# Kernel optimization log

Measured on AMD Instinct MI355X. Metric: run time of the kernel, lower is better.

The kernel has to match this reference:

```python
import jax, jax.numpy as jnp
import numpy as np

DXV, DRUGV = 10000, 3000
DXANC, DRUGANC = 2000, 600
A = 8            # max ancestors per leaf
ONTOD = 128; EHRD = 128; ATTND = 128; PTATTND = 128; DPL = 500
B, T, DXN, DRUGN = 64, 20, 30, 30


def _l2norm(x):
    n = jnp.sqrt(jnp.sum(x * x, axis=-1, keepdims=True))
    return x / jnp.maximum(n, 1e-12)


def _onto_emb(emb, leaves, ancestors, aW, ab, cW, cb):
    # GRAM-style ontology attention: per leaf, attend over its ancestor set.
    le = emb[leaves]          # (V, A, ONTOD)
    ae = emb[ancestors]       # (V, A, ONTOD)
    s = jnp.tanh(jnp.concatenate([le, ae], -1) @ aW + ab) @ cW + cb  # (V, A, 1)
    attn = jax.nn.softmax(s, axis=1)
    out = jnp.sum(attn * ae, axis=1)                                 # (V, ONTOD)
    pad = jnp.zeros((1, out.shape[1]), out.dtype)                    # padding row at idx V
    return jnp.concatenate([out, pad], axis=0)


def setup_inputs() -> dict:
    key = jax.random.key(0)
    ks = jax.random.split(key, 24)
    s = 0.02
    dxseqs = jax.random.randint(ks[0], (B, T, DXN), 0, DXV + 1)
    drugseqs = jax.random.randint(ks[1], (B, T, DRUGN), 0, DRUGV + 1)
    dx_onehot = jax.random.uniform(ks[2], (T, B, DXV), dtype=jnp.float32)
    drug_onehot = jax.random.uniform(ks[3], (T, B, DRUGV), dtype=jnp.float32)
    dx_leaves = jnp.broadcast_to(jnp.arange(DXV)[:, None], (DXV, A))
    dx_ancestors = jax.random.randint(ks[4], (DXV, A), 0, DXV + DXANC).at[:, 0].set(jnp.arange(DXV))
    drug_leaves = jnp.broadcast_to(jnp.arange(DRUGV)[:, None], (DRUGV, A))
    drug_ancestors = jax.random.randint(ks[5], (DRUGV, A), 0, DRUGV + DRUGANC).at[:, 0].set(jnp.arange(DRUGV))
    ehr_dx_emb = (jax.random.normal(ks[6], (DXV + 1, EHRD)) * s).at[DXV].set(0.0)
    ehr_drug_emb = (jax.random.normal(ks[7], (DRUGV + 1, EHRD)) * s).at[DRUGV].set(0.0)
    return {
        "dxseqs": dxseqs, "drugseqs": drugseqs,
        "dx_onehot": dx_onehot, "drug_onehot": drug_onehot,
        "dx_leaves": dx_leaves, "dx_ancestors": dx_ancestors,
        "drug_leaves": drug_leaves, "drug_ancestors": drug_ancestors,
        "dx_onto_emb": jax.random.normal(ks[8], (DXV + DXANC, ONTOD)) * s,
        "dx_onto_aW": jax.random.normal(ks[9], (2 * ONTOD, ATTND)) * s,
        "dx_onto_ab": jnp.zeros((ATTND,)),
        "dx_onto_cW": jax.random.normal(ks[10], (ATTND, 1)) * s,
        "dx_onto_cb": jnp.zeros((1,)),
        "drug_onto_emb": jax.random.normal(ks[11], (DRUGV + DRUGANC, ONTOD)) * s,
        "drug_onto_aW": jax.random.normal(ks[12], (2 * ONTOD, ATTND)) * s,
        "drug_onto_ab": jnp.zeros((ATTND,)),
        "drug_onto_cW": jax.random.normal(ks[13], (ATTND, 1)) * s,
        "drug_onto_cb": jnp.zeros((1,)),
        "ehr_dx_emb": ehr_dx_emb, "ehr_drug_emb": ehr_drug_emb,
        "co_W": jax.random.normal(ks[14], (EHRD, DXV + DRUGV)) * s,
        "co_b": jnp.zeros((DXV + DRUGV,)),
        "attn_W": jax.random.normal(ks[15], (2 * ONTOD + 2 * EHRD, PTATTND)) * s,
        "attn_b": jnp.zeros((PTATTND,)),
        "comb_W": jax.random.normal(ks[16], (PTATTND, 1)) * s,
        "comb_b": jnp.zeros((1,)),
        "dp_W": jax.random.normal(ks[17], (ONTOD + EHRD, DPL)) * s,
        "dp_b": jnp.zeros((DPL,)),
        "read_W": jax.random.normal(ks[18], (ONTOD + EHRD, 1)) * s,
        "read_b": jnp.zeros((1,)),
    }


def reference(dxseqs, drugseqs, dx_onehot, drug_onehot,
              dx_leaves, dx_ancestors, drug_leaves, drug_ancestors,
              dx_onto_emb, dx_onto_aW, dx_onto_ab, dx_onto_cW, dx_onto_cb,
              drug_onto_emb, drug_onto_aW, drug_onto_ab, drug_onto_cW, drug_onto_cb,
              ehr_dx_emb, ehr_drug_emb, co_W, co_b,
              attn_W, attn_b, comb_W, comb_b, dp_W, dp_b, read_W, read_b):
    dxALL = _onto_emb(dx_onto_emb, dx_leaves, dx_ancestors, dx_onto_aW, dx_onto_ab, dx_onto_cW, dx_onto_cb)      # (DXV+1, ONTOD)
    drugALL = _onto_emb(drug_onto_emb, drug_leaves, drug_ancestors, drug_onto_aW, drug_onto_ab, drug_onto_cW, drug_onto_cb)
    dxE = ehr_dx_emb[dxseqs]                                # (B,T,DXN,EHRD)
    drugE = ehr_drug_emb[drugseqs]                          # (B,T,DRUGN,EHRD)
    EHREmb = jnp.concatenate([dxE, drugE], axis=2)          # (B,T,N,EHRD)
    ontoEmb = jnp.concatenate([dxALL[dxseqs], drugALL[drugseqs]], axis=2)  # (B,T,N,ONTOD)
    EHRVEmb = _l2norm(jnp.sum(dxE, axis=2)) + _l2norm(jnp.sum(drugE, axis=2))  # (B,T,EHRD)
    dxontoV = jnp.einsum('tbv,vd->btd', dx_onehot, dxALL[:-1])
    drugontoV = jnp.einsum('tbv,vd->btd', drug_onehot, drugALL[:-1])
    cooccurU = jax.nn.softmax(EHRVEmb @ co_W + co_b, axis=2)               # (B,T,DXV+DRUGV)
    vonehot = jnp.concatenate([jnp.transpose(dx_onehot, (1, 0, 2)),
                               jnp.transpose(drug_onehot, (1, 0, 2))], axis=2)
    cooccur_loss = -jnp.mean(jnp.sum(vonehot * jnp.log(cooccurU), axis=(1, 2)))
    ontoV = _l2norm(dxontoV) + _l2norm(drugontoV)
    vs = jnp.concatenate([ontoV, EHRVEmb], axis=2)          # (B,T,ONTOD+EHRD)
    dxdrug = jnp.concatenate([EHREmb, ontoEmb], axis=3)     # (B,T,N,EHRD+ONTOD)
    N = dxdrug.shape[2]
    vs_rep = jnp.broadcast_to(vs[:, :, None, :], (vs.shape[0], vs.shape[1], N, vs.shape[2]))
    attnInput = jnp.concatenate([vs_rep, dxdrug], axis=3)   # (B,T,N,2*ONTOD+2*EHRD)
    pre = jnp.tanh(attnInput @ attn_W + attn_b) @ comb_W + comb_b          # (B,T,N,1)
    attn = jax.nn.softmax(pre, axis=2)
    vs2 = jnp.sum(attn * dxdrug, axis=2)                    # (B,T,EHRD+ONTOD)
    vs_dp = _l2norm(vs2)
    DP_result = jax.nn.softmax(jnp.tanh(vs_dp) @ dp_W + dp_b, axis=2)
    read_result = jax.nn.sigmoid(vs_dp @ read_W + read_b)
    return (read_result, DP_result, cooccur_loss * 10.0)
```

## Files before the change

kernel.cpp:

```cpp
#include <hip/hip_runtime.h>
#include <hip/hip_bf16.h>
#include <math.h>

#define BB 64
#define TT 20
#define BT 1280
#define DXV 10000
#define DRUGV 3000
#define COV 13000
#define DPL 500
#define KC 40

typedef __attribute__((ext_vector_type(8))) short short8v;
typedef __attribute__((ext_vector_type(4))) float f32x4;

__device__ __forceinline__ unsigned short f2bf(float f) {
  __hip_bfloat16 h = __float2bfloat16(f);
  return *reinterpret_cast<unsigned short*>(&h);
}

__global__ __launch_bounds__(256, 4) void k_onto(
    const float* __restrict__ emb, const int* __restrict__ leaves, const int* __restrict__ anc,
    const float* __restrict__ aW, const float* __restrict__ ab, const float* __restrict__ cW,
    float* __restrict__ out)
{
  __shared__ __align__(16) float xe[4][128];
  __shared__ __align__(16) float xa[4][8][128];
  __shared__ float part[4][8][2];
  __shared__ float sv[32];
  const int tid = threadIdx.x;
  const int v0 = blockIdx.x * 4;

  for (int i = tid; i < 4*128; i += 256) {
    const int lv = i >> 7, d = i & 127;
    xe[lv][d] = emb[leaves[(v0 + lv)*8] * 128 + d];
  }
  for (int i = tid; i < 32*128; i += 256) {
    const int row = i >> 7, d = i & 127;
    xa[row >> 3][row & 7][d] = emb[anc[(v0 + (row >> 3))*8 + (row & 7)] * 128 + d];
  }
  __syncthreads();

  const int j = tid & 127, half = tid >> 7;

  float ld[4];
  { const float abj = ab[j]; ld[0] = ld[1] = ld[2] = ld[3] = abj; }
  for (int k0 = 0; k0 < 128; k0 += 4) {
    const float w0 = aW[(k0+0)*128 + j];
    const float w1 = aW[(k0+1)*128 + j];
    const float w2 = aW[(k0+2)*128 + j];
    const float w3 = aW[(k0+3)*128 + j];
    #pragma unroll
    for (int lv = 0; lv < 4; ++lv) {
      const float4 x4 = *reinterpret_cast<const float4*>(&xe[lv][k0]);
      ld[lv] = fmaf(x4.x, w0, fmaf(x4.y, w1, fmaf(x4.z, w2, fmaf(x4.w, w3, ld[lv]))));
    }
  }

  float acc[4][4];
  #pragma unroll
  for (int lv = 0; lv < 4; ++lv)
    #pragma unroll
    for (int ai = 0; ai < 4; ++ai) acc[lv][ai] = ld[lv];
  for (int k0 = 0; k0 < 128; k0 += 4) {
    const float w0 = aW[(128+k0+0)*128 + j];
    const float w1 = aW[(128+k0+1)*128 + j];
    const float w2 = aW[(128+k0+2)*128 + j];
    const float w3 = aW[(128+k0+3)*128 + j];
    float4 es[16];
    #pragma unroll
    for (int lv = 0; lv < 4; ++lv)
      #pragma unroll
      for (int ai = 0; ai < 4; ++ai)
        es[lv*4 + ai] = *reinterpret_cast<const float4*>(&xa[lv][half + 2*ai][k0]);
    #pragma unroll
    for (int lv = 0; lv < 4; ++lv)
      #pragma unroll
      for (int ai = 0; ai < 4; ++ai) {
        const float4 e4 = es[lv*4 + ai];
        acc[lv][ai] = fmaf(e4.x, w0, fmaf(e4.y, w1, fmaf(e4.z, w2, fmaf(e4.w, w3, acc[lv][ai]))));
      }
  }

  {
    const float cwj = cW[j];
    #pragma unroll
    for (int lv = 0; lv < 4; ++lv)
      #pragma unroll
      for (int ai = 0; ai < 4; ++ai) {
        float p = tanhf(acc[lv][ai]) * cwj;
        for (int off = 32; off; off >>= 1) p += __shfl_down(p, off);
        if ((tid & 63) == 0) part[lv][half + 2*ai][(tid >> 6) & 1] = p;
      }
  }
  __syncthreads();
  if (tid < 32) sv[tid] = part[tid >> 3][tid & 7][0] + part[tid >> 3][tid & 7][1];
  __syncthreads();
  if (tid < 4) {
    float m = -1e30f;
    #pragma unroll
    for (int a = 0; a < 8; ++a) m = fmaxf(m, sv[tid*8 + a]);
    float e[8], ssum = 0.f;
    #pragma unroll
    for (int a = 0; a < 8; ++a) { e[a] = __expf(sv[tid*8 + a] - m); ssum += e[a]; }
    const float inv = 1.f / ssum;
    #pragma unroll
    for (int a = 0; a < 8; ++a) sv[tid*8 + a] = e[a] * inv;
  }
  __syncthreads();
  #pragma unroll
  for (int it = 0; it < 2; ++it) {
    const int i = it*256 + tid;
    const int lv = i >> 7, d = i & 127;
    float o = 0.f;
    #pragma unroll
    for (int a = 0; a < 8; ++a) o += sv[lv*8 + a] * xa[lv][a][d];
    out[(v0 + lv)*128 + d] = o;
  }
}

__global__ __launch_bounds__(128) void k_ehr(
    const int* __restrict__ dxs, const int* __restrict__ drs,
    const float* __restrict__ edx, const float* __restrict__ edr,
    float* __restrict__ vs)
{
  const int bt = blockIdx.x, d = threadIdx.x;
  float sdx = 0.f, sdr = 0.f;
  for (int n = 0; n < 30; ++n) sdx += edx[dxs[bt*30 + n]*128 + d];
  for (int n = 0; n < 30; ++n) sdr += edr[drs[bt*30 + n]*128 + d];
  __shared__ float red[2][2];
  float p1 = sdx*sdx, p2 = sdr*sdr;
  for (int off = 32; off; off >>= 1) { p1 += __shfl_down(p1, off); p2 += __shfl_down(p2, off); }
  if ((d & 63) == 0) { red[0][d>>6] = p1; red[1][d>>6] = p2; }
  __syncthreads();
  const float n1 = sqrtf(red[0][0] + red[0][1]);
  const float n2 = sqrtf(red[1][0] + red[1][1]);
  vs[bt*256 + 128 + d] = sdx / fmaxf(n1, 1e-12f) + sdr / fmaxf(n2, 1e-12f);
}

__global__ __launch_bounds__(256, 4) void k_einsum(
    const float* __restrict__ oneh, const float* __restrict__ tabl,
    float* __restrict__ outp, int V, int vcount)
{
  __shared__ __align__(16) float As[32][KC];
  __shared__ __align__(16) float Bs[KC][128];
  const int tid = threadIdx.x;
  const int rbase = blockIdx.x * 32;
  const int vbase = blockIdx.y * vcount;
  const int cg = tid & 31, rg = tid >> 5;
  const int d0 = cg * 4, r0 = rg * 4;
  float acc[4][4];
  #pragma unroll
  for (int r = 0; r < 4; ++r)
    #pragma unroll
    for (int q = 0; q < 4; ++q) acc[r][q] = 0.f;

  for (int c0 = 0; c0 < vcount; c0 += KC) {
    __syncthreads();
    for (int i = tid; i < 320; i += 256) {
      const int r = i / 10, q = i % 10;
      const int row = rbase + r;
      const int b = row / TT, t = row % TT;
      *reinterpret_cast<float4*>(&As[r][q*4]) =
          *reinterpret_cast<const float4*>(&oneh[(t*BB + b)*V + vbase + c0 + q*4]);
    }
    for (int i = tid; i < 1280; i += 256) {
      const int rr = i >> 5, q = i & 31;
      *reinterpret_cast<float4*>(&Bs[rr][q*4]) =
          *reinterpret_cast<const float4*>(&tabl[(vbase + c0 + rr)*128 + q*4]);
    }
    __syncthreads();
    #pragma unroll
    for (int kk = 0; kk < KC; kk += 4) {
      const float4 b0 = *reinterpret_cast<const float4*>(&Bs[kk+0][d0]);
      const float4 b1 = *reinterpret_cast<const float4*>(&Bs[kk+1][d0]);
      const float4 b2 = *reinterpret_cast<const float4*>(&Bs[kk+2][d0]);
      const float4 b3 = *reinterpret_cast<const float4*>(&Bs[kk+3][d0]);
      float4 a4[4];
      #pragma unroll
      for (int r = 0; r < 4; ++r) a4[r] = *reinterpret_cast<const float4*>(&As[r0 + r][kk]);
      #pragma unroll
      for (int r = 0; r < 4; ++r) {
        acc[r][0] = fmaf(a4[r].x, b0.x, fmaf(a4[r].y, b1.x, fmaf(a4[r].z, b2.x, fmaf(a4[r].w, b3.x, acc[r][0]))));
        acc[r][1] = fmaf(a4[r].x, b0.y, fmaf(a4[r].y, b1.y, fmaf(a4[r].z, b2.y, fmaf(a4[r].w, b3.y, acc[r][1]))));
        acc[r][2] = fmaf(a4[r].x, b0.z, fmaf(a4[r].y, b1.z, fmaf(a4[r].z, b2.z, fmaf(a4[r].w, b3.z, acc[r][2]))));
        acc[r][3] = fmaf(a4[r].x, b0.w, fmaf(a4[r].y, b1.w, fmaf(a4[r].z, b2.w, fmaf(a4[r].w, b3.w, acc[r][3]))));
      }
    }
  }
  #pragma unroll
  for (int r = 0; r < 4; ++r) {
    const int row = rbase + r0 + r;
    #pragma unroll
    for (int q = 0; q < 4; ++q)
      atomicAdd(&outp[row*128 + d0 + q], acc[r][q]);
  }
}

__global__ __launch_bounds__(128) void k_vs(
    const float* __restrict__ dxo, const float* __restrict__ dro, float* __restrict__ vs)
{
  const int bt = blockIdx.x, d = threadIdx.x;
  const float a = dxo[bt*128 + d], b = dro[bt*128 + d];
  __shared__ float red[2][2];
  float p1 = a*a, p2 = b*b;
  for (int off = 32; off; off >>= 1) { p1 += __shfl_down(p1, off); p2 += __shfl_down(p2, off); }
  if ((d & 63) == 0) { red[0][d>>6] = p1; red[1][d>>6] = p2; }
  __syncthreads();
  const float n1 = sqrtf(red[0][0] + red[0][1]);
  const float n2 = sqrtf(red[1][0] + red[1][1]);
  vs[bt*256 + d] = a / fmaxf(n1, 1e-12f) + b / fmaxf(n2, 1e-12f);
}

__global__ __launch_bounds__(256) void k_cvtco(
    const float* __restrict__ coW, unsigned short* __restrict__ coWbT)
{
  __shared__ float t[32][129];
  const int v0 = blockIdx.x * 32;
  const int tid = threadIdx.x;
  for (int i = tid; i < 128*32; i += 256) {
    const int k = i >> 5, v = i & 31;
    if (v0 + v < COV) t[v][k] = coW[k*COV + v0 + v];
  }
  __syncthreads();
  for (int i = tid; i < 32*128; i += 256) {
    const int v = i >> 7, k = i & 127;
    if (v0 + v < COV) coWbT[(v0 + v)*128 + k] = f2bf(t[v][k]);
  }
}

__global__ __launch_bounds__(256, 4) void k_cooc(
    const float* __restrict__ vs, const unsigned short* __restrict__ coWbT,
    const float* __restrict__ cob,
    const float* __restrict__ dxoh, const float* __restrict__ droh,
    float* __restrict__ es_g, float* __restrict__ od_g, float* __restrict__ os_g)
{
  __shared__ __align__(16) unsigned short Xa[32*128];
  __shared__ float l_es[32], l_od[32], l_os[32];
  const int tid = threadIdx.x;
  const int rbase = blockIdx.x * 32;
  const int nbase = blockIdx.y * 512;
  char* xb = reinterpret_cast<char*>(Xa);

  if (tid < 32) { l_es[tid] = 0.f; l_od[tid] = 0.f; l_os[tid] = 0.f; }
  for (int i = tid; i < 32*32; i += 256) {
    const int r = i >> 5, q = i & 31;
    const float4 v = *reinterpret_cast<const float4*>(&vs[(rbase + r)*256 + 128 + q*4]);
    ushort4 h;
    h.x = f2bf(v.x); h.y = f2bf(v.y); h.z = f2bf(v.z); h.w = f2bf(v.w);
    const int byte = (r*256 + q*8) ^ ((r & 7) << 4);
    *reinterpret_cast<ushort4*>(xb + byte) = h;
  }
  __syncthreads();

  const int lane = tid & 63, w = tid >> 6;
  const int l15 = lane & 15, kg = lane >> 4;
  const int nw = nbase + w*128;
  f32x4 acc[2][8];
  #pragma unroll
  for (int mt = 0; mt < 2; ++mt)
    #pragma unroll
    for (int nt = 0; nt < 8; ++nt) acc[mt][nt] = f32x4{0.f, 0.f, 0.f, 0.f};

  #pragma unroll
  for (int kt = 0; kt < 4; ++kt) {
    short8v a[2];
    #pragma unroll
    for (int mt = 0; mt < 2; ++mt) {
      const int row = mt*16 + l15;
      a[mt] = *reinterpret_cast<const short8v*>(xb + ((row*256 + kt*64 + kg*16) ^ ((row & 7) << 4)));
    }
    #pragma unroll
    for (int nt = 0; nt < 8; ++nt) {
      int ncol = nw + nt*16 + l15;
      if (ncol > COV - 1) ncol = COV - 1;
      const short8v b = *reinterpret_cast<const short8v*>(
          reinterpret_cast<const char*>(coWbT) + ncol*256 + kt*64 + kg*16);
      acc[0][nt] = __builtin_amdgcn_mfma_f32_16x16x32_bf16(a[0], b, acc[0][nt], 0, 0, 0);
      acc[1][nt] = __builtin_amdgcn_mfma_f32_16x16x32_bf16(a[1], b, acc[1][nt], 0, 0, 0);
    }
  }

  #pragma unroll
  for (int mt = 0; mt < 2; ++mt) {
    #pragma unroll
    for (int r = 0; r < 4; ++r) {
      const int lrow = mt*16 + kg*4 + r;
      const int grow = rbase + lrow;
      const int b_ = grow / TT, t_ = grow % TT;
      float es_a = 0.f, od_a = 0.f, os_a = 0.f;
      #pragma unroll
      for (int nt = 0; nt < 8; ++nt) {
        const int v = nw + nt*16 + l15;
        if (v < COV) {
          const float lgv = acc[mt][nt][r] + cob[v];
          const float oh = (v < DXV) ? dxoh[(t_*BB + b_)*DXV + v]
                                     : droh[(t_*BB + b_)*DRUGV + (v - DXV)];
          es_a += __expf(lgv);
          od_a = fmaf(oh, lgv, od_a);
          os_a += oh;
        }
      }
      #pragma unroll
      for (int off = 1; off < 16; off <<= 1) {
        es_a += __shfl_xor(es_a, off);
        od_a += __shfl_xor(od_a, off);
        os_a += __shfl_xor(os_a, off);
      }
      if (l15 == 0) {
        atomicAdd(&l_es[lrow], es_a);
        atomicAdd(&l_od[lrow], od_a);
        atomicAdd(&l_os[lrow], os_a);
      }
    }
  }
  __syncthreads();
  if (tid < 32) {
    atomicAdd(&es_g[rbase + tid], l_es[tid]);
    atomicAdd(&od_g[rbase + tid], l_od[tid]);
    atomicAdd(&os_g[rbase + tid], l_os[tid]);
  }
}

__global__ __launch_bounds__(256) void k_loss(
    const float* __restrict__ es_g, const float* __restrict__ od_g, const float* __restrict__ os_g,
    float* __restrict__ out)
{
  const int tid = threadIdx.x;
  float a = 0.f;
  for (int r = tid; r < BT; r += 256)
    a += logf(es_g[r]) * os_g[r] - od_g[r];
  __shared__ float red[4];
  for (int off = 32; off; off >>= 1) a += __shfl_down(a, off);
  if ((tid & 63) == 0) red[tid >> 6] = a;
  __syncthreads();
  if (tid == 0) out[0] = (red[0] + red[1] + red[2] + red[3]) * (10.f / (float)BB);
}

__global__ __launch_bounds__(128) void k_cvtw(
    const float* __restrict__ aW, unsigned short* __restrict__ aWbT)
{
  const int k = blockIdx.x, n = threadIdx.x;
  aWbT[n*256 + k] = f2bf(aW[(256 + k)*128 + n]);
}

__global__ __launch_bounds__(256, 4) void k_attn(
    const int* __restrict__ dxs, const int* __restrict__ drs,
    const float* __restrict__ edx, const float* __restrict__ edr,
    const float* __restrict__ dxALL, const float* __restrict__ drugALL,
    const float* __restrict__ vs, const float* __restrict__ aW,
    const float* __restrict__ ab, const float* __restrict__ cWc,
    const unsigned short* __restrict__ aWbT,
    float* __restrict__ vsdp)
{
  __shared__ __align__(16) unsigned short X2[64*256];
  __shared__ __align__(16) float vrow[256];
  __shared__ float bp[2][128];
  __shared__ float base[128];
  __shared__ float sattn[64];
  __shared__ int codes[60];
  __shared__ float red[4];
  const int tid = threadIdx.x;
  const int bt = blockIdx.x;
  char* x2b = reinterpret_cast<char*>(X2);

  if (tid < 64) sattn[tid] = 0.f;
  if (tid < 60) codes[tid] = (tid < 30) ? dxs[bt*30 + tid] : drs[bt*30 + tid - 30];
  vrow[tid] = vs[bt*256 + tid];
  __syncthreads();

  for (int idx = tid; idx < 60*64; idx += 256) {
    const int n = idx >> 6, q = idx & 63;
    const float* src = (q < 32) ? ((n < 30) ? edx : edr)
                                : ((n < 30) ? dxALL : drugALL);
    const float4 v = *reinterpret_cast<const float4*>(&src[codes[n]*128 + (q & 31)*4]);
    ushort4 h;
    h.x = f2bf(v.x); h.y = f2bf(v.y); h.z = f2bf(v.z); h.w = f2bf(v.w);
    const int byte = (n*512 + q*8) ^ ((n & 7) << 4);
    *reinterpret_cast<ushort4*>(x2b + byte) = h;
  }
  for (int idx = tid; idx < 4*64; idx += 256) {
    const int n = 60 + (idx >> 6), q = idx & 63;
    *reinterpret_cast<ushort4*>(x2b + ((n*512 + q*8) ^ ((n & 7) << 4))) = ushort4{0,0,0,0};
  }

  const int j = tid & 127, ng = tid >> 7;
  {
    float p = 0.f;
    const int kb = ng * 128;
    for (int k0 = 0; k0 < 128; k0 += 4) {
      const float4 v4 = *reinterpret_cast<const float4*>(&vrow[kb + k0]);
      p = fmaf(v4.x, aW[(kb+k0+0)*128 + j],
          fmaf(v4.y, aW[(kb+k0+1)*128 + j],
          fmaf(v4.z, aW[(kb+k0+2)*128 + j],
          fmaf(v4.w, aW[(kb+k0+3)*128 + j], p))));
    }
    bp[ng][j] = p;
  }
  __syncthreads();
  if (tid < 128) base[tid] = ab[tid] + bp[0][tid] + bp[1][tid];
  __syncthreads();

  const int lane = tid & 63, w = tid >> 6;
  const int l15 = lane & 15, kg = lane >> 4;
  f32x4 acc[4][2];
  #pragma unroll
  for (int mt = 0; mt < 4; ++mt)
    #pragma unroll
    for (int ns = 0; ns < 2; ++ns) acc[mt][ns] = f32x4{0.f, 0.f, 0.f, 0.f};

  #pragma unroll
  for (int kt = 0; kt < 8; ++kt) {
    short8v a[4];
    #pragma unroll
    for (int mt = 0; mt < 4; ++mt) {
      const int row = mt*16 + l15;
      const int byte = (row*512 + kt*64 + kg*16) ^ ((row & 7) << 4);
      a[mt] = *reinterpret_cast<const short8v*>(x2b + byte);
    }
    #pragma unroll
    for (int ns = 0; ns < 2; ++ns) {
      const int ncol = (2*w + ns)*16 + l15;
      const short8v b = *reinterpret_cast<const short8v*>(
          reinterpret_cast<const char*>(aWbT) + ncol*512 + kt*64 + kg*16);
      #pragma unroll
      for (int mt = 0; mt < 4; ++mt)
        acc[mt][ns] = __builtin_amdgcn_mfma_f32_16x16x32_bf16(a[mt], b, acc[mt][ns], 0, 0, 0);
    }
  }

  {
    const int c0 = 2*w*16 + l15, c1 = c0 + 16;
    const float b0 = base[c0], b1 = base[c1];
    const float cw0 = cWc[c0], cw1 = cWc[c1];
    #pragma unroll
    for (int mt = 0; mt < 4; ++mt) {
      #pragma unroll
      for (int r = 0; r < 4; ++r) {
        float p = fmaf(cw0, tanhf(b0 + acc[mt][0][r]), cw1 * tanhf(b1 + acc[mt][1][r]));
        p += __shfl_xor(p, 1); p += __shfl_xor(p, 2);
        p += __shfl_xor(p, 4); p += __shfl_xor(p, 8);
        const int row = mt*16 + kg*4 + r;
        if (l15 == 0 && row < 60) atomicAdd(&sattn[row], p);
      }
    }
  }
  __syncthreads();

  if (tid < 64) {
    const float v = (tid < 60) ? sattn[tid] : -1e30f;
    float m = v;
    for (int off = 32; off; off >>= 1) m = fmaxf(m, __shfl_xor(m, off));
    const float e = (tid < 60) ? __expf(v - m) : 0.f;
    float s = e;
    for (int off = 32; off; off >>= 1) s += __shfl_xor(s, off);
    if (tid < 60) sattn[tid] = e / s;
  }
  __syncthreads();

  float acc2 = 0.f;
  {
    const int d2 = tid * 2;
    for (int n = 0; n < 60; ++n) {
      const unsigned short u = *reinterpret_cast<const unsigned short*>(
          x2b + ((n*512 + d2) ^ ((n & 7) << 4)));
      acc2 = fmaf(sattn[n], __uint_as_float(((unsigned)u) << 16), acc2);
    }
  }
  float p = acc2 * acc2;
  for (int off = 32; off; off >>= 1) p += __shfl_down(p, off);
  if ((tid & 63) == 0) red[tid >> 6] = p;
  __syncthreads();
  const float nrm = sqrtf(red[0] + red[1] + red[2] + red[3]);
  vsdp[bt*256 + tid] = acc2 / fmaxf(nrm, 1e-12f);
}

__global__ __launch_bounds__(256) void k_out(
    const float* __restrict__ vsdp, const float* __restrict__ dpW, const float* __restrict__ dpb,
    const float* __restrict__ rW, const float* __restrict__ rb, float* __restrict__ out)
{
  __shared__ __align__(16) float tv[256];
  __shared__ float lg[512];
  __shared__ float red[4], red2[4], red3[4];
  const int bt = blockIdx.x, tid = threadIdx.x;
  const float vraw = vsdp[bt*256 + tid];
  tv[tid] = tanhf(vraw);
  __syncthreads();
  for (int l = tid; l < DPL; l += 256) {
    float a = dpb[l];
    for (int k0 = 0; k0 < 256; k0 += 4) {
      const float4 t4 = *reinterpret_cast<const float4*>(&tv[k0]);
      a = fmaf(t4.x, dpW[(k0+0)*DPL + l],
          fmaf(t4.y, dpW[(k0+1)*DPL + l],
          fmaf(t4.z, dpW[(k0+2)*DPL + l],
          fmaf(t4.w, dpW[(k0+3)*DPL + l], a))));
    }
    lg[l] = a;
  }
  __syncthreads();
  float m = -1e30f;
  for (int l = tid; l < DPL; l += 256) m = fmaxf(m, lg[l]);
  for (int off = 32; off; off >>= 1) m = fmaxf(m, __shfl_xor(m, off));
  if ((tid & 63) == 0) red[tid >> 6] = m;
  __syncthreads();
  m = fmaxf(fmaxf(red[0], red[1]), fmaxf(red[2], red[3]));
  float s = 0.f;
  for (int l = tid; l < DPL; l += 256) s += __expf(lg[l] - m);
  for (int off = 32; off; off >>= 1) s += __shfl_xor(s, off);
  if ((tid & 63) == 0) red2[tid >> 6] = s;
  __syncthreads();
  s = red2[0] + red2[1] + red2[2] + red2[3];
  const float inv = 1.f / s;
  for (int l = tid; l < DPL; l += 256) out[BT + bt*DPL + l] = __expf(lg[l] - m) * inv;
  float p = vraw * rW[tid];
  for (int off = 32; off; off >>= 1) p += __shfl_down(p, off);
  if ((tid & 63) == 0) red3[tid >> 6] = p;
  __syncthreads();
  if (tid == 0) {
    const float tot = red3[0] + red3[1] + red3[2] + red3[3] + rb[0];
    out[bt] = 1.f / (1.f + __expf(-tot));
  }
}

extern "C" void kernel_launch(void* const* d_in, const int* in_sizes, int n_in,
                              void* d_out, int out_size, void* d_ws, size_t ws_size,
                              hipStream_t stream) {
  const int*   dxseqs = (const int*)d_in[0];
  const int*   drseqs = (const int*)d_in[1];
  const float* dxoh   = (const float*)d_in[2];
  const float* droh   = (const float*)d_in[3];
  const int*   dxlv   = (const int*)d_in[4];
  const int*   dxan   = (const int*)d_in[5];
  const int*   drlv   = (const int*)d_in[6];
  const int*   dran   = (const int*)d_in[7];
  const float* dxoe   = (const float*)d_in[8];
  const float* dxaW   = (const float*)d_in[9];
  const float* dxab   = (const float*)d_in[10];
  const float* dxcW   = (const float*)d_in[11];
  const float* droe   = (const float*)d_in[13];
  const float* draW   = (const float*)d_in[14];
  const float* drab   = (const float*)d_in[15];
  const float* drcW   = (const float*)d_in[16];
  const float* edx    = (const float*)d_in[18];
  const float* edr    = (const float*)d_in[19];
  const float* coW    = (const float*)d_in[20];
  const float* cob    = (const float*)d_in[21];
  const float* aW     = (const float*)d_in[22];
  const float* ab     = (const float*)d_in[23];
  const float* cWc    = (const float*)d_in[24];
  const float* dpW    = (const float*)d_in[26];
  const float* dpb    = (const float*)d_in[27];
  const float* rW     = (const float*)d_in[28];
  const float* rb     = (const float*)d_in[29];
  float* out = (float*)d_out;

  float* ws      = (float*)d_ws;
  float* dxALL   = ws;
  float* drugALL = dxALL   + 10001*128;
  float* vsbuf   = drugALL + 3001*128;
  float* dxoV    = vsbuf   + 1280*256;
  float* droV    = dxoV    + 1280*128;
  float* vsdp    = droV    + 1280*128;
  float* es_g    = vsdp    + 1280*256;
  float* od_g    = es_g    + 1280;
  float* os_g    = od_g    + 1280;
  unsigned short* aWbT  = (unsigned short*)(os_g + 1280);
  unsigned short* coWbT = aWbT + 128*256;

  hipMemsetAsync(dxALL + 10000*128, 0, 128*sizeof(float), stream);
  hipMemsetAsync(drugALL + 3000*128, 0, 128*sizeof(float), stream);
  hipMemsetAsync(dxoV, 0, 2*1280*128*sizeof(float), stream);
  hipMemsetAsync(es_g, 0, 3*1280*sizeof(float), stream);

  k_cvtw<<<256, 128, 0, stream>>>(aW, aWbT);
  k_cvtco<<<(COV + 31)/32, 256, 0, stream>>>(coW, coWbT);
  k_onto<<<DXV/4,  256, 0, stream>>>(dxoe, dxlv, dxan, dxaW, dxab, dxcW, dxALL);
  k_onto<<<DRUGV/4,256, 0, stream>>>(droe, drlv, dran, draW, drab, drcW, drugALL);
  k_ehr<<<BT, 128, 0, stream>>>(dxseqs, drseqs, edx, edr, vsbuf);
  k_einsum<<<dim3(BT/32, 10), 256, 0, stream>>>(dxoh, dxALL, dxoV, DXV, 1000);
  k_einsum<<<dim3(BT/32, 5),  256, 0, stream>>>(droh, drugALL, droV, DRUGV, 600);
  k_vs<<<BT, 128, 0, stream>>>(dxoV, droV, vsbuf);
  k_cooc<<<dim3(BT/32, 26), 256, 0, stream>>>(vsbuf, coWbT, cob, dxoh, droh, es_g, od_g, os_g);
  k_loss<<<1, 256, 0, stream>>>(es_g, od_g, os_g, out + BT + BT*DPL);
  k_attn<<<BT, 256, 0, stream>>>(dxseqs, drseqs, edx, edr, dxALL, drugALL, vsbuf, aW, ab, cWc, aWbT, vsdp);
  k_out<<<BT, 256, 0, stream>>>(vsdp, dpW, dpb, rW, rb, out);
}
```

Measured before the change: 608.1 us.

## Split einsum K across more blocks, write partials, prefetch tiles in registers

The onehot-by-table einsum kernels now split the vocabulary dimension into 25 and 15 slices instead of 10 and 5, which gives more blocks. Each block writes its partial result with plain float4 stores into a per-slice buffer instead of doing atomicAdd. The k_vs kernel then sums the slices, and the output memset is dropped. The main loop also prefetches the next global tiles into registers while the current tile is being computed, a software pipeline. The cost is extra workspace and extra reads in k_vs.

```diff
diff --git a/kernel.cpp b/kernel.cpp
--- a/kernel.cpp
+++ b/kernel.cpp
@@ -10,6 +10,8 @@
 #define COV 13000
 #define DPL 500
 #define KC 40
+#define NSDX 25
+#define NSDR 15
 
 typedef __attribute__((ext_vector_type(8))) short short8v;
 typedef __attribute__((ext_vector_type(4))) float f32x4;
@@ -140,36 +142,60 @@
 
 __global__ __launch_bounds__(256, 4) void k_einsum(
     const float* __restrict__ oneh, const float* __restrict__ tabl,
-    float* __restrict__ outp, int V, int vcount)
+    float* __restrict__ outs, int V, int vcount)
 {
   __shared__ __align__(16) float As[32][KC];
   __shared__ __align__(16) float Bs[KC][128];
   const int tid = threadIdx.x;
   const int rbase = blockIdx.x * 32;
   const int vbase = blockIdx.y * vcount;
+  float* __restrict__ myout = outs + blockIdx.y * (BT*128);
   const int cg = tid & 31, rg = tid >> 5;
   const int d0 = cg * 4, r0 = rg * 4;
+
+  float4 ra[2], rb[5];
   float acc[4][4];
   #pragma unroll
   for (int r = 0; r < 4; ++r)
     #pragma unroll
     for (int q = 0; q < 4; ++q) acc[r][q] = 0.f;
 
+  #define LOADRS(c0)                                                           \
+    {                                                                          \
+      _Pragma("unroll")                                                        \
+      for (int u = 0; u < 2; ++u) {                                            \
+        const int i = tid + 256*u;                                             \
+        if (i < 320) {                                                         \
+          const int r = i / 10, q = i % 10;                                    \
+          const int row = rbase + r;                                           \
+          const int b = row / TT, t = row % TT;                                \
+          ra[u] = *reinterpret_cast<const float4*>(                            \
+              &oneh[(t*BB + b)*V + vbase + (c0) + q*4]);                       \
+        }                                                                      \
+      }                                                                        \
+      _Pragma("unroll")                                                        \
+      for (int u = 0; u < 5; ++u) {                                            \
+        const int i = tid + 256*u;                                             \
+        rb[u] = *reinterpret_cast<const float4*>(                              \
+            &tabl[(vbase + (c0) + (i >> 5))*128 + (i & 31)*4]);                \
+      }                                                                        \
+    }
+
+  LOADRS(0)
   for (int c0 = 0; c0 < vcount; c0 += KC) {
     __syncthreads();
-    for (int i = tid; i < 320; i += 256) {
-      const int r = i / 10, q = i % 10;
-      const int row = rbase + r;
-      const int b = row / TT, t = row % TT;
-      *reinterpret_cast<float4*>(&As[r][q*4]) =
-          *reinterpret_cast<const float4*>(&oneh[(t*BB + b)*V + vbase + c0 + q*4]);
-    }
-    for (int i = tid; i < 1280; i += 256) {
-      const int rr = i >> 5, q = i & 31;
-      *reinterpret_cast<float4*>(&Bs[rr][q*4]) =
-          *reinterpret_cast<const float4*>(&tabl[(vbase + c0 + rr)*128 + q*4]);
+    #pragma unroll
+    for (int u = 0; u < 2; ++u) {
+      const int i = tid + 256*u;
+      if (i < 320) *reinterpret_cast<float4*>(&As[i / 10][(i % 10)*4]) = ra[u];
+    }
+    #pragma unroll
+    for (int u = 0; u < 5; ++u) {
+      const int i = tid + 256*u;
+      *reinterpret_cast<float4*>(&Bs[i >> 5][(i & 31)*4]) = rb[u];
     }
     __syncthreads();
+    if (c0 + KC < vcount) LOADRS(c0 + KC)
     #pragma unroll
     for (int kk = 0; kk < KC; kk += 4) {
       const float4 b0 = *reinterpret_cast<const float4*>(&Bs[kk+0][d0]);
@@ -190,18 +216,21 @@
   }
   #pragma unroll
   for (int r = 0; r < 4; ++r) {
-    const int row = rbase + r0 + r;
-    #pragma unroll
-    for (int q = 0; q < 4; ++q)
-      atomicAdd(&outp[row*128 + d0 + q], acc[r][q]);
-  }
+    float4 o; o.x = acc[r][0]; o.y = acc[r][1]; o.z = acc[r][2]; o.w = acc[r][3];
+    *reinterpret_cast<float4*>(&myout[(rbase + r0 + r)*128 + d0]) = o;
+  }
+  #undef LOADRS
 }
 
 __global__ __launch_bounds__(128) void k_vs(
-    const float* __restrict__ dxo, const float* __restrict__ dro, float* __restrict__ vs)
+    const float* __restrict__ dxoVs, const float* __restrict__ droVs, float* __restrict__ vs)
 {
   const int bt = blockIdx.x, d = threadIdx.x;
-  const float a = dxo[bt*128 + d], b = dro[bt*128 + d];
+  float a = 0.f, b = 0.f;
+  #pragma unroll
+  for (int s = 0; s < NSDX; ++s) a += dxoVs[s*(BT*128) + bt*128 + d];
+  #pragma unroll
+  for (int s = 0; s < NSDR; ++s) b += droVs[s*(BT*128) + bt*128 + d];
   __shared__ float red[2][2];
   float p1 = a*a, p2 = b*b;
   for (int off = 32; off; off >>= 1) { p1 += __shfl_down(p1, off); p2 += __shfl_down(p2, off); }
@@ -558,18 +587,17 @@
   float* dxALL   = ws;
   float* drugALL = dxALL   + 10001*128;
   float* vsbuf   = drugALL + 3001*128;
-  float* dxoV    = vsbuf   + 1280*256;
-  float* droV    = dxoV    + 1280*128;
-  float* vsdp    = droV    + 1280*128;
+  float* vsdp    = vsbuf   + 1280*256;
   float* es_g    = vsdp    + 1280*256;
   float* od_g    = es_g    + 1280;
   float* os_g    = od_g    + 1280;
   unsigned short* aWbT  = (unsigned short*)(os_g + 1280);
   unsigned short* coWbT = aWbT + 128*256;
+  float* dxoVs   = (float*)(coWbT + 13000*128);
+  float* droVs   = dxoVs + NSDX*BT*128;
 
   hipMemsetAsync(dxALL + 10000*128, 0, 128*sizeof(float), stream);
   hipMemsetAsync(drugALL + 3000*128, 0, 128*sizeof(float), stream);
-  hipMemsetAsync(dxoV, 0, 2*1280*128*sizeof(float), stream);
   hipMemsetAsync(es_g, 0, 3*1280*sizeof(float), stream);
 
   k_cvtw<<<256, 128, 0, stream>>>(aW, aWbT);
@@ -577,9 +605,9 @@
   k_onto<<<DXV/4,  256, 0, stream>>>(dxoe, dxlv, dxan, dxaW, dxab, dxcW, dxALL);
   k_onto<<<DRUGV/4,256, 0, stream>>>(droe, drlv, dran, draW, drab, drcW, drugALL);
   k_ehr<<<BT, 128, 0, stream>>>(dxseqs, drseqs, edx, edr, vsbuf);
-  k_einsum<<<dim3(BT/32, 10), 256, 0, stream>>>(dxoh, dxALL, dxoV, DXV, 1000);
-  k_einsum<<<dim3(BT/32, 5),  256, 0, stream>>>(droh, drugALL, droV, DRUGV, 600);
-  k_vs<<<BT, 128, 0, stream>>>(dxoV, droV, vsbuf);
+  k_einsum<<<dim3(BT/32, NSDX), 256, 0, stream>>>(dxoh, dxALL, dxoVs, DXV, DXV/NSDX);
+  k_einsum<<<dim3(BT/32, NSDR), 256, 0, stream>>>(droh, drugALL, droVs, DRUGV, DRUGV/NSDR);
+  k_vs<<<BT, 128, 0, stream>>>(dxoVs, droVs, vsbuf);
   k_cooc<<<dim3(BT/32, 26), 256, 0, stream>>>(vsbuf, coWbT, cob, dxoh, droh, es_g, od_g, os_g);
   k_loss<<<1, 256, 0, stream>>>(es_g, od_g, os_g, out + BT + BT*DPL);
   k_attn<<<BT, 256, 0, stream>>>(dxseqs, drseqs, edx, edr, dxALL, drugALL, vsbuf, aW, ab, cWc, aWbT, vsdp);
```

Result: no change. 613.6 us (+0.9%).
